# Kernel optimization log

Measured on AMD Instinct MI355X. Metric: run time of the kernel, lower is better.

Reference implementation:

```python
import jax, jax.numpy as jnp
import numpy as np

B, NF, G, H, W = 4, 64, 8, 96, 96
K, KK = 3, 9
CG = NF // G  # channels per deformable group


def _conv3(x, w, b):
    # 3x3 conv, stride 1, pad 1, NCHW/OIHW
    y = jax.lax.conv_general_dilated(x, w, (1, 1), ((1, 1), (1, 1)),
                                     dimension_numbers=('NCHW', 'OIHW', 'NCHW'))
    return y + b[None, :, None, None]


def _lrelu(x):
    return jnp.where(x >= 0, x, 0.1 * x)


def _up2(x):
    # bilinear x2 upsample, align_corners=False (PyTorch semantics: src clamped at 0, indices clamped at n-1)
    def up_axis(x, axis):
        n = x.shape[axis]
        src = jnp.maximum((jnp.arange(2 * n, dtype=jnp.float32) + 0.5) / 2.0 - 0.5, 0.0)
        i0 = jnp.floor(src).astype(jnp.int32)
        i1 = jnp.minimum(i0 + 1, n - 1)
        t = (src - i0.astype(jnp.float32))
        x0 = jnp.take(x, i0, axis=axis)
        x1 = jnp.take(x, i1, axis=axis)
        shp = [1] * x.ndim
        shp[axis] = 2 * n
        t = t.reshape(shp)
        return x0 * (1.0 - t) + x1 * t
    return up_axis(up_axis(x, 2), 3)


def _dcn(x, off_feat, w_om, b_om, w_d, b_d):
    # Modulated deformable conv (DCNv2, separate offset input), 3x3, stride 1, pad 1, dil 1,
    # conv groups = 1, deformable groups = G.
    b, c, h, w = x.shape
    om = _conv3(off_feat, w_om, b_om)                     # [B, 3*G*KK, H, W]
    o_y, o_x, m = jnp.split(om, 3, axis=1)                # each [B, G*KK, H, W]
    off_y = o_y.reshape(b, G, KK, h, w)
    off_x = o_x.reshape(b, G, KK, h, w)
    mask = jax.nn.sigmoid(m).reshape(b, G, KK, h, w)

    dy = (jnp.arange(KK, dtype=jnp.float32) // K - 1.0)   # [-1,-1,-1,0,0,0,1,1,1]
    dx = (jnp.arange(KK, dtype=jnp.float32) % K - 1.0)
    ys = jnp.arange(h, dtype=jnp.float32)
    xs = jnp.arange(w, dtype=jnp.float32)
    # sampling positions: [B, G, KK, H, W]
    py = off_y + ys[None, None, None, :, None] + dy[None, None, :, None, None]
    px = off_x + xs[None, None, None, None, :] + dx[None, None, :, None, None]

    y0f = jnp.floor(py); x0f = jnp.floor(px)
    ty = py - y0f; tx = px - x0f
    y0 = y0f.astype(jnp.int32); x0 = x0f.astype(jnp.int32)
    y1 = y0 + 1; x1 = x0 + 1

    xg = x.reshape(b, G, CG, h * w)  # per-deformable-group channels

    def samp(iy, ix):
        valid = ((iy >= 0) & (iy < h) & (ix >= 0) & (ix < w)).astype(x.dtype)  # [B,G,KK,H,W]
        idx = jnp.clip(iy, 0, h - 1) * w + jnp.clip(ix, 0, w - 1)
        idxf = idx.reshape(b, G, 1, KK * h * w)
        v = jnp.take_along_axis(xg, jnp.broadcast_to(idxf, (b, G, CG, KK * h * w)), axis=3)
        return v.reshape(b, G, CG, KK, h, w) * valid[:, :, None]

    w00 = ((1 - ty) * (1 - tx))[:, :, None]
    w01 = ((1 - ty) * tx)[:, :, None]
    w10 = (ty * (1 - tx))[:, :, None]
    w11 = (ty * tx)[:, :, None]
    cols = (samp(y0, x0) * w00 + samp(y0, x1) * w01 +
            samp(y1, x0) * w10 + samp(y1, x1) * w11)
    cols = cols * mask[:, :, None]                        # modulation
    cols = cols.reshape(b, c, KK, h, w)
    out = jnp.einsum('bckhw,ock->bohw', cols, w_d.reshape(c, c, KK))
    return out + b_d[None, :, None, None]


def setup_inputs() -> dict:
    key = jax.random.key(0)
    ks = jax.random.split(key, 20)
    s = 0.05
    inp = {
        'src0': jax.random.normal(ks[0], (B, NF, H, W), jnp.float32),
        'src1': jax.random.normal(ks[1], (B, NF, H, W), jnp.float32),
        'last_offset': jax.random.normal(ks[2], (B, NF, H // 2, W // 2), jnp.float32),
        'last_feature': jax.random.normal(ks[3], (B, NF, H // 2, W // 2), jnp.float32),
        'w_off1': jax.random.normal(ks[4], (NF, 2 * NF, 3, 3), jnp.float32) * s,
        'b_off1': jax.random.normal(ks[5], (NF,), jnp.float32) * s,
        'w_off2': jax.random.normal(ks[6], (NF, 2 * NF, 3, 3), jnp.float32) * s,
        'b_off2': jax.random.normal(ks[7], (NF,), jnp.float32) * s,
        'w_off3': jax.random.normal(ks[8], (NF, NF, 3, 3), jnp.float32) * s,
        'b_off3': jax.random.normal(ks[9], (NF,), jnp.float32) * s,
        'w_om': jax.random.normal(ks[10], (3 * G * KK, NF, 3, 3), jnp.float32) * s,
        'b_om': jax.random.normal(ks[11], (3 * G * KK,), jnp.float32) * s,
        'w_dcn': jax.random.normal(ks[12], (NF, NF, 3, 3), jnp.float32) * s,
        'b_dcn': jax.random.normal(ks[13], (NF,), jnp.float32) * s,
        'w_fea': jax.random.normal(ks[14], (NF, 2 * NF, 3, 3), jnp.float32) * s,
        'b_fea': jax.random.normal(ks[15], (NF,), jnp.float32) * s,
    }
    return inp


def reference(src0, src1, last_offset, last_feature,
              w_off1, b_off1, w_off2, b_off2, w_off3, b_off3,
              w_om, b_om, w_dcn, b_dcn, w_fea, b_fea):
    offset = _lrelu(_conv3(jnp.concatenate([src0, src1], axis=1), w_off1, b_off1))
    lo = _up2(last_offset)
    offset = _lrelu(_conv3(jnp.concatenate([offset, lo * 2.0], axis=1), w_off2, b_off2))
    offset = _lrelu(_conv3(offset, w_off3, b_off3))
    feature = _dcn(src0, offset, w_om, b_om, w_dcn, b_dcn)
    lf = _up2(last_feature)
    feature = _conv3(jnp.concatenate([feature, lf], axis=1), w_fea, b_fea)
    feature = _lrelu(feature)
    return (offset, feature)
```

## Files before the change

### kernel.cpp

```cpp
#include <hip/hip_runtime.h>
#include <hip/hip_fp16.h>
#include <math.h>

typedef __attribute__((ext_vector_type(8))) short bf16x8;
typedef __attribute__((ext_vector_type(8))) _Float16 half8;
typedef __attribute__((ext_vector_type(4))) float f32x4;
typedef __attribute__((ext_vector_type(4))) int int4v;

#define GL_LDS16(g, l) __builtin_amdgcn_global_load_lds( \
    (const __attribute__((address_space(1))) void*)(g), \
    (__attribute__((address_space(3))) void*)(l), 16, 0, 0)

__device__ __forceinline__ ushort f2bf(float f) {
    union { float f; unsigned u; } v; v.f = f;
    unsigned r = (v.u + 0x7fffu + ((v.u >> 16) & 1u)) >> 16;
    return (ushort)r;
}
__device__ __forceinline__ float bf2f(ushort h) {
    union { unsigned u; float f; } v; v.u = ((unsigned)h) << 16;
    return v.f;
}

__device__ __forceinline__ void prep_one(const float* __restrict__ w,
        ushort* __restrict__ wp, int u, int Cin, int CoutR, int CoutP) {
    int oc = u % CoutP; int t = u / CoutP;
    int kg = t & 3; t >>= 2;
    int kk = t % 9; int cc = t / 9;
    alignas(16) ushort tmp[8];
    for (int j = 0; j < 8; ++j) {
        int c = cc * 32 + kg * 8 + j;
        float v = (oc < CoutR) ? w[((size_t)oc * Cin + c) * 9 + kk] : 0.f;
        tmp[j] = f2bf(v);
    }
    *(int4v*)(wp + (size_t)u * 8) = *(int4v*)tmp;
}

__global__ __launch_bounds__(256) void pack_combo_k(
        const float* __restrict__ s0, const float* __restrict__ s1,
        const float* __restrict__ lo, const float* __restrict__ lf,
        const float* __restrict__ w1, const float* __restrict__ w2,
        const float* __restrict__ w3, const float* __restrict__ wom,
        const float* __restrict__ wd, const float* __restrict__ wf,
        const float* __restrict__ bom,
        ushort* __restrict__ xin1, ushort* __restrict__ xin2,
        ushort* __restrict__ xin4, ushort* __restrict__ xg1,
        ushort* __restrict__ w1p, ushort* __restrict__ w2p,
        ushort* __restrict__ w3p, ushort* __restrict__ womp,
        ushort* __restrict__ wdp, ushort* __restrict__ wfp,
        float* __restrict__ bpp, float* __restrict__ zg) {
    int b = blockIdx.y;
    int z = blockIdx.z;
    int px = blockIdx.x * 64 + (threadIdx.x & 63);
    int u = threadIdx.x >> 6;
    if (z == 0) {
        for (int half = 0; half < 2; ++half) {
            int cg = u + half * 4;
            float vals[16];
            alignas(16) ushort tmp[16];
            for (int i = 0; i < 16; ++i) {
                int c = cg * 16 + i;
                float v = (c < 64) ? s0[((size_t)(b * 64 + c)) * 9216 + px]
                                   : s1[((size_t)(b * 64 + c - 64)) * 9216 + px];
                vals[i] = v;
                tmp[i] = f2bf(v);
            }
            ushort* dst = xin1 + ((size_t)(b * 9216) + px) * 128 + cg * 16;
            *(int4v*)dst = *(int4v*)&tmp[0];
            *(int4v*)(dst + 8) = *(int4v*)&tmp[8];
            if (half == 0) {
                alignas(16) __half th[16];
                for (int i = 0; i < 16; ++i) th[i] = __float2half(vals[i]);
                ushort* gdst = xg1 + (((size_t)(b * 8 + cg * 2) * 9216) + px) * 8;
                *(int4v*)gdst = *(int4v*)&th[0];
                *(int4v*)(gdst + 9216 * 8) = *(int4v*)&th[8];
            }
        }
    } else if (z < 3) {
        const float* in = (z == 1) ? lo : lf;
        float scale = (z == 1) ? 2.0f : 1.0f;
        ushort* xo = (z == 1) ? xin2 : xin4;
        int y = px / 96, x = px % 96;
        float sy = fmaxf(y * 0.5f - 0.25f, 0.f);
        float sx = fmaxf(x * 0.5f - 0.25f, 0.f);
        int y0 = (int)sy, x0 = (int)sx;
        float ty = sy - (float)y0, tx = sx - (float)x0;
        int y1 = min(y0 + 1, 47), x1 = min(x0 + 1, 47);
        alignas(16) ushort tmp[16];
        for (int i = 0; i < 16; ++i) {
            int c = u * 16 + i;
            const float* p = in + ((size_t)(b * 64 + c)) * 2304;
            float v00 = p[y0 * 48 + x0], v01 = p[y0 * 48 + x1];
            float v10 = p[y1 * 48 + x0], v11 = p[y1 * 48 + x1];
            float v = (v00 * (1.f - tx) + v01 * tx) * (1.f - ty)
                    + (v10 * (1.f - tx) + v11 * tx) * ty;
            tmp[i] = f2bf(v * scale);
        }
        ushort* dst = xo + ((size_t)(b * 9216) + px) * 128 + 64 + u * 16;
        *(int4v*)dst = *(int4v*)&tmp[0];
        *(int4v*)(dst + 8) = *(int4v*)&tmp[8];
    } else {
        int uu = (blockIdx.x + 144 * blockIdx.y) * 256 + threadIdx.x;
        if (uu < 9216) prep_one(w1, w1p, uu, 128, 64, 64);
        else if (uu < 18432) prep_one(w2, w2p, uu - 9216, 128, 64, 64);
        else if (uu < 23040) prep_one(w3, w3p, uu - 18432, 64, 64, 64);
        else if (uu < 43776) {
            int v = uu - 23040;
            int ocp = v % 288; int t = v / 288;
            int kg = t & 3; t >>= 2;
            int kk = t % 9; int cc = t / 9;
            int t3 = ocp & 3, gkkp = ocp >> 2;
            alignas(16) ushort tmp[8];
            for (int j = 0; j < 8; ++j) {
                int c = cc * 32 + kg * 8 + j;
                float vv = (t3 < 3)
                    ? wom[((size_t)(t3 * 72 + gkkp) * 64 + c) * 9 + kk] : 0.f;
                tmp[j] = f2bf(vv);
            }
            *(int4v*)(womp + (size_t)v * 8) = *(int4v*)tmp;
        } else if (uu < 48384) {
            int v = uu - 43776;
            int oc = v & 63; int gkk = v >> 6;
            int g = gkk / 9, kk = gkk % 9;
            alignas(16) __half tmp[8];
            for (int j = 0; j < 8; ++j)
                tmp[j] = __float2half(wd[((size_t)oc * 64 + g * 8 + j) * 9 + kk]);
            *(int4v*)(wdp + (size_t)v * 8) = *(int4v*)tmp;
        } else if (uu < 57600) prep_one(wf, wfp, uu - 48384, 128, 64, 64);
        else if (uu < 57888) {
            int ocp = uu - 57600; int t3 = ocp & 3, gkkp = ocp >> 2;
            bpp[ocp] = (t3 < 3) ? bom[t3 * 72 + gkkp] : 0.f;
        } else if (uu < 57904) zg[uu - 57888] = 0.f;
    }
}

template<int CIN, int MT, int NZ, bool LRELU, bool ST_F32, bool ST_CHL>
__global__ __launch_bounds__(256, 4) void conv_mfma_k(
        const ushort* __restrict__ xin,
        const ushort* __restrict__ wp,
        const float* __restrict__ bias,
        float* __restrict__ outf,
        ushort* __restrict__ chl,
        const ushort* __restrict__ zg,
        int CoutR, int CoutP, int ochs, int ocoff) {
    constexpr int SL = CIN / 64;
    constexpr int OCN = MT * 16;
    __shared__ ushort s_act[SL][7200];

    int tid = threadIdx.x;
    int wv = tid >> 6, ln = tid & 63;
    int l15 = ln & 15, l4 = ln >> 4;

    constexpr int TOTAL = 144 * 4 * NZ;
    constexpr int CHUNK = TOTAL / 8;
    int bid = blockIdx.x;
    int nid = (bid & 7) * CHUNK + (bid >> 3);
    int zc = nid % NZ; int r1 = nid / NZ;
    int tile = r1 % 144; int b = r1 / 144;
    int bx = (tile % 12) * 8, by = (tile / 12) * 8;
    int oc0 = zc * OCN;

    int px_l = wv * 16 + l15;
    int py = px_l >> 3, pxx = px_l & 7;
    int b_base = (py * 10 + pxx) * 72 + l4 * 8;

    const ushort* wlane = wp + ((size_t)l4 * CoutP + oc0 + l15) * 8;

    f32x4 acc[MT];
#pragma unroll
    for (int mt = 0; mt < MT; ++mt) acc[mt] = (f32x4){0.f, 0.f, 0.f, 0.f};

    auto STAGE = [&](int sl, int buf) {
        for (int i = tid; i < 900; i += 256) {
            int p = i / 9, q = i - p * 9;
            int gy = by + (p / 10) - 1, gx = bx + (p % 10) - 1;
            const ushort* src = zg;
            if (q < 8 && (unsigned)gy < 96u && (unsigned)gx < 96u)
                src = xin + ((size_t)(b * 9216 + gy * 96 + gx) * CIN
                             + sl * 64 + q * 8);
            GL_LDS16(src, s_act[buf] + (size_t)i * 8);
        }
    };

    STAGE(0, 0);
    __syncthreads();
#pragma unroll
    for (int sl = 0; sl < SL; ++sl) {
        if (sl + 1 < SL) STAGE(sl + 1, (sl + 1) & 1);
#pragma unroll
        for (int cc2 = 0; cc2 < 2; ++cc2) {
#pragma unroll
            for (int kk = 0; kk < 9; ++kk) {
                bf16x8 bfrag = *(const bf16x8*)(s_act[sl & (SL - 1)] + b_base +
                                   ((kk / 3) * 10 + (kk % 3)) * 72 + cc2 * 32);
#pragma unroll
                for (int mt = 0; mt < MT; ++mt) {
                    bf16x8 af = *(const bf16x8*)(wlane +
                        ((size_t)((sl * 2 + cc2) * 36 + kk * 4) * CoutP + mt * 16) * 8);
                    acc[mt] = __builtin_amdgcn_mfma_f32_16x16x32_bf16(
                        af, bfrag, acc[mt], 0, 0, 0);
                }
            }
        }
        if (sl + 1 < SL) __syncthreads();
    }

    int gy = by + py, gx = bx + pxx;
    size_t pxg = (size_t)b * 9216 + gy * 96 + gx;
#pragma unroll
    for (int mt = 0; mt < MT; ++mt) {
        int ocb = oc0 + mt * 16 + l4 * 4;
        ushort hb[4];
#pragma unroll
        for (int r = 0; r < 4; ++r) {
            int oc = ocb + r;
            float v = acc[mt][r] + ((oc < CoutR) ? bias[oc] : 0.f);
            if (LRELU) v = (v >= 0.f) ? v : 0.1f * v;
            hb[r] = f2bf(v);
            if (ST_F32 && oc < CoutR)
                outf[((size_t)b * CoutR + oc) * 9216 + gy * 96 + gx] = v;
        }
        if (ST_CHL && ocb < CoutR) {
            uint2 pk;
            pk.x = (uint)hb[0] | ((uint)hb[1] << 16);
            pk.y = (uint)hb[2] | ((uint)hb[3] << 16);
            *(uint2*)(chl + pxg * ochs + ocoff + ocb) = pk;
        }
    }
}

__global__ __launch_bounds__(128, 4) void dcn_fused_k(
        const ushort* __restrict__ xg1,
        const ushort* __restrict__ om,
        const ushort* __restrict__ wdp,
        const float* __restrict__ bd, ushort* __restrict__ chl) {
    __shared__ float s_red[64][17];
    int tid = threadIdx.x;
    int kq = tid >> 6, ln = tid & 63;
    int l15 = ln & 15, l4 = ln >> 4;
    int bid = blockIdx.x;
    int nid = (bid & 7) * 288 + (bid >> 3);
    int pxb = nid % 576; int b = nid / 576;
    int px = pxb * 16 + l15;
    int y = px / 96, xx = px % 96;

    f32x4 acc[4];
#pragma unroll
    for (int mt = 0; mt < 4; ++mt) acc[mt] = (f32x4){0.f, 0.f, 0.f, 0.f};
    const ushort* omp_ = om + ((size_t)b * 9216 + px) * 288 + kq * 144;

    uint2 ovv[9];
#pragma unroll
    for (int s = 0; s < 9; ++s)
        ovv[s] = *(const uint2*)(omp_ + s * 16 + l4 * 4);

    int4v Abuf[2][4];
    float cwbuf[2][4];

    auto PREP = [&](int s, int4v* A, float* cw) {
        int gkk = kq * 36 + s * 4 + l4;
        int g = gkk / 9, kk = gkk - g * 9;
        union { uint2 u; ushort us[4]; } ov; ov.u = ovv[s];
        float oy = bf2f(ov.us[0]), ox = bf2f(ov.us[1]);
        float mm = 1.f / (1.f + __expf(-bf2f(ov.us[2])));
        float py = oy + (float)(y + kk / 3 - 1);
        float pxf = ox + (float)(xx + kk % 3 - 1);
        float yf = floorf(py), xf = floorf(pxf);
        float fy = py - yf, fx = pxf - xf;
        int iy0 = (int)yf, ix0 = (int)xf;
        int iy1 = iy0 + 1, ix1 = ix0 + 1;
        float vy0 = ((unsigned)iy0 < 96u) ? 1.f : 0.f;
        float vy1 = ((unsigned)iy1 < 96u) ? 1.f : 0.f;
        float vx0 = ((unsigned)ix0 < 96u) ? 1.f : 0.f;
        float vx1 = ((unsigned)ix1 < 96u) ? 1.f : 0.f;
        int r0 = min(max(iy0, 0), 95), r1 = min(max(iy1, 0), 95);
        int lb = min(max(ix0, 0), 94);
        float h0 = (float)min(max(ix0 - lb, 0), 1);
        float h1 = (float)min(max(ix1 - lb, 0), 1);
        float wx0 = (1.f - fx) * vx0, wx1 = fx * vx1;
        float xw0 = wx0 * (1.f - h0) + wx1 * (1.f - h1);
        float xw1 = wx0 * h0 + wx1 * h1;
        float rw0 = (1.f - fy) * vy0 * mm, rw1 = fy * vy1 * mm;
        cw[0] = rw0 * xw0; cw[1] = rw0 * xw1;
        cw[2] = rw1 * xw0; cw[3] = rw1 * xw1;
        const ushort* gp = xg1 + ((size_t)(b * 8 + g) * 9216) * 8;
        const ushort* p0 = gp + ((size_t)(r0 * 96 + lb)) * 8;
        const ushort* p1 = gp + ((size_t)(r1 * 96 + lb)) * 8;
        A[0] = *(const int4v*)p0;
        A[1] = *(const int4v*)(p0 + 8);
        A[2] = *(const int4v*)p1;
        A[3] = *(const int4v*)(p1 + 8);
    };

    PREP(0, Abuf[0], cwbuf[0]);
#pragma unroll
    for (int s = 0; s < 9; ++s) {
        if (s + 1 < 9) PREP(s + 1, Abuf[(s + 1) & 1], cwbuf[(s + 1) & 1]);
        const int4v* A = Abuf[s & 1];
        const float* cw = cwbuf[s & 1];
        union { int4v v; __half2 h2[4]; } a0, a1, b0, b1;
        a0.v = A[0]; a1.v = A[1]; b0.v = A[2]; b1.v = A[3];
        __half2 w0 = __float2half2_rn(cw[0]);
        __half2 w1 = __float2half2_rn(cw[1]);
        __half2 w2 = __float2half2_rn(cw[2]);
        __half2 w3 = __float2half2_rn(cw[3]);
        union { __half2 h2[4]; half8 v; } bu;
#pragma unroll
        for (int j = 0; j < 4; ++j) {
            __half2 t = __hmul2(a0.h2[j], w0);
            t = __hfma2(a1.h2[j], w1, t);
            t = __hfma2(b0.h2[j], w2, t);
            t = __hfma2(b1.h2[j], w3, t);
            bu.h2[j] = t;
        }
        int gkk = kq * 36 + s * 4 + l4;
#pragma unroll
        for (int mt = 0; mt < 4; ++mt) {
            half8 af = *(const half8*)(wdp +
                ((size_t)gkk * 64 + mt * 16 + l15) * 8);
            acc[mt] = __builtin_amdgcn_mfma_f32_16x16x32_f16(
                af, bu.v, acc[mt], 0, 0, 0);
        }
    }

    if (kq) {
#pragma unroll
        for (int mt = 0; mt < 4; ++mt)
#pragma unroll
            for (int r = 0; r < 4; ++r)
                s_red[ln][mt * 4 + r] = acc[mt][r];
    }
    __syncthreads();
    if (!kq) {
        size_t pb = (size_t)b * 9216 + px;
#pragma unroll
        for (int mt = 0; mt < 4; ++mt) {
            ushort hb[4];
#pragma unroll
            for (int r = 0; r < 4; ++r) {
                int oc = mt * 16 + l4 * 4 + r;
                float v = acc[mt][r] + s_red[ln][mt * 4 + r] + bd[oc];
                hb[r] = f2bf(v);
            }
            uint2 pk;
            pk.x = (uint)hb[0] | ((uint)hb[1] << 16);
            pk.y = (uint)hb[2] | ((uint)hb[3] << 16);
            *(uint2*)(chl + pb * 128 + mt * 16 + l4 * 4) = pk;
        }
    }
}

extern "C" void kernel_launch(void* const* d_in, const int* in_sizes, int n_in,
                              void* d_out, int out_size, void* d_ws, size_t ws_size,
                              hipStream_t stream) {
    const float* src0  = (const float*)d_in[0];
    const float* src1  = (const float*)d_in[1];
    const float* l_off = (const float*)d_in[2];
    const float* l_fea = (const float*)d_in[3];
    const float* w1 = (const float*)d_in[4];   const float* b1 = (const float*)d_in[5];
    const float* w2 = (const float*)d_in[6];   const float* b2 = (const float*)d_in[7];
    const float* w3 = (const float*)d_in[8];   const float* b3 = (const float*)d_in[9];
    const float* wom = (const float*)d_in[10]; const float* bom = (const float*)d_in[11];
    const float* wd = (const float*)d_in[12];  const float* bd = (const float*)d_in[13];
    const float* wf = (const float*)d_in[14];  const float* bf = (const float*)d_in[15];

    char* W = (char*)d_ws;
    ushort* xin1 = (ushort*)(W + 0);
    ushort* xin2 = (ushort*)(W + 9437184);
    ushort* xoff = (ushort*)(W + 9437184);
    ushort* xin3 = (ushort*)(W + 18874368);
    ushort* omb  = (ushort*)(W + 23592960);
    ushort* xin4 = (ushort*)(W + 44826624);
    ushort* xg1  = (ushort*)(W + 54263808);
    ushort* w1p  = (ushort*)(W + 58982400);
    ushort* w2p  = (ushort*)(W + 59129856);
    ushort* w3p  = (ushort*)(W + 59277312);
    ushort* womp = (ushort*)(W + 59351040);
    ushort* wdp  = (ushort*)(W + 59682816);
    ushort* wfp  = (ushort*)(W + 59756544);
    float*  bpp  = (float*)(W + 59904000);
    float*  zgrd = (float*)(W + 59905152);

    float* out_off = (float*)d_out;
    float* out_fea = out_off + (size_t)4 * 64 * 9216;

    pack_combo_k<<<dim3(144, 4, 4), 256, 0, stream>>>(
        src0, src1, l_off, l_fea, w1, w2, w3, wom, wd, wf, bom,
        xin1, xin2, xin4, xg1, w1p, w2p, w3p, womp, wdp, wfp, bpp, zgrd);

    const ushort* zg = (const ushort*)zgrd;
    conv_mfma_k<128, 2, 2, true, false, true><<<1152, 256, 0, stream>>>(
        xin1, w1p, b1, nullptr, xin2, zg, 64, 64, 128, 0);
    conv_mfma_k<128, 2, 2, true, false, true><<<1152, 256, 0, stream>>>(
        xin2, w2p, b2, nullptr, xin3, zg, 64, 64, 64, 0);
    conv_mfma_k<64, 2, 2, true, true, true><<<1152, 256, 0, stream>>>(
        xin3, w3p, b3, out_off, xoff, zg, 64, 64, 64, 0);
    conv_mfma_k<64, 6, 3, false, false, true><<<1728, 256, 0, stream>>>(
        xoff, womp, bpp, nullptr, omb, zg, 288, 288, 288, 0);
    dcn_fused_k<<<2304, 128, 0, stream>>>(xg1, omb, wdp, bd, xin4);
    conv_mfma_k<128, 2, 2, true, true, false><<<1152, 256, 0, stream>>>(
        xin4, wfp, bf, out_fea, nullptr, zg, 64, 64, 0, 0);
}
```

Measured before the change: 145.1 us.

## Fuse offset/mask conv into deformable conv kernel, drop om intermediate

Removes the separate conv that produced the 288-channel offset/mask tensor. Each DCN block now stages its 3x18 halo of the offset features into LDS and computes the offsets and masks with MFMA before sampling. This saves one kernel launch plus the write and re-read of the large om buffer. In exchange, weights are read from global memory per block with no reuse across blocks, register pressure rises (launch bounds cut to 3 blocks), and the per-block compute grows.

New measurement: 131.8 us. 9.2% less time.

```diff
diff --git a/kernel.cpp b/kernel.cpp
--- a/kernel.cpp
+++ b/kernel.cpp
@@ -228,11 +228,15 @@
     }
 }
 
-__global__ __launch_bounds__(128, 4) void dcn_fused_k(
+__global__ __launch_bounds__(128, 3) void dcn_fused_k(
+        const ushort* __restrict__ xoff,
         const ushort* __restrict__ xg1,
-        const ushort* __restrict__ om,
+        const ushort* __restrict__ womp,
+        const float* __restrict__ bpp,
         const ushort* __restrict__ wdp,
-        const float* __restrict__ bd, ushort* __restrict__ chl) {
+        const float* __restrict__ bd, ushort* __restrict__ chl,
+        const ushort* __restrict__ zg) {
+    __shared__ ushort s_x[3456];
     __shared__ float s_red[64][17];
     int tid = threadIdx.x;
     int kq = tid >> 6, ln = tid & 63;
@@ -240,18 +244,48 @@
     int bid = blockIdx.x;
     int nid = (bid & 7) * 288 + (bid >> 3);
     int pxb = nid % 576; int b = nid / 576;
-    int px = pxb * 16 + l15;
-    int y = px / 96, xx = px % 96;
+    int px0 = pxb * 16;
+    int px = px0 + l15;
+    int y = px0 / 96, x0 = px0 % 96;
+    int xx = x0 + l15;
+
+    for (int i = tid; i < 432; i += 128) {
+        int P = i >> 3, s8 = i & 7;
+        int q = s8 ^ (P & 7);
+        int ry = y - 1 + P / 18, rx = x0 - 1 + P % 18;
+        const ushort* src = zg;
+        if ((unsigned)ry < 96u && (unsigned)rx < 96u)
+            src = xoff + (((size_t)b * 9216 + ry * 96 + rx) * 64 + q * 8);
+        GL_LDS16(src, s_x + (size_t)i * 8);
+    }
+    __syncthreads();
+
+    f32x4 aom[9];
+#pragma unroll
+    for (int s = 0; s < 9; ++s) aom[s] = (f32x4){0.f, 0.f, 0.f, 0.f};
+#pragma unroll
+    for (int kk = 0; kk < 9; ++kk) {
+        int ky = kk / 3, kx = kk % 3;
+#pragma unroll
+        for (int cc = 0; cc < 2; ++cc) {
+            int P = ky * 18 + l15 + kx;
+            int c8 = cc * 4 + l4;
+            bf16x8 bfrag = *(const bf16x8*)(s_x +
+                ((size_t)(P * 8 + (c8 ^ (P & 7)))) * 8);
+#pragma unroll
+            for (int s = 0; s < 9; ++s) {
+                bf16x8 af = *(const bf16x8*)(womp +
+                    ((size_t)(((cc * 9 + kk) * 4 + l4) * 288)
+                     + kq * 144 + s * 16 + l15) * 8);
+                aom[s] = __builtin_amdgcn_mfma_f32_16x16x32_bf16(
+                    af, bfrag, aom[s], 0, 0, 0);
+            }
+        }
+    }
 
     f32x4 acc[4];
 #pragma unroll
     for (int mt = 0; mt < 4; ++mt) acc[mt] = (f32x4){0.f, 0.f, 0.f, 0.f};
-    const ushort* omp_ = om + ((size_t)b * 9216 + px) * 288 + kq * 144;
-
-    uint2 ovv[9];
-#pragma unroll
-    for (int s = 0; s < 9; ++s)
-        ovv[s] = *(const uint2*)(omp_ + s * 16 + l4 * 4);
 
     int4v Abuf[2][4];
     float cwbuf[2][4];
@@ -259,9 +293,10 @@
     auto PREP = [&](int s, int4v* A, float* cw) {
         int gkk = kq * 36 + s * 4 + l4;
         int g = gkk / 9, kk = gkk - g * 9;
-        union { uint2 u; ushort us[4]; } ov; ov.u = ovv[s];
-        float oy = bf2f(ov.us[0]), ox = bf2f(ov.us[1]);
-        float mm = 1.f / (1.f + __expf(-bf2f(ov.us[2])));
+        int bofs = kq * 144 + s * 16 + l4 * 4;
+        float oy = aom[s][0] + bpp[bofs];
+        float ox = aom[s][1] + bpp[bofs + 1];
+        float mm = 1.f / (1.f + __expf(-(aom[s][2] + bpp[bofs + 2])));
         float py = oy + (float)(y + kk / 3 - 1);
         float pxf = ox + (float)(xx + kk % 3 - 1);
         float yf = floorf(py), xf = floorf(pxf);
@@ -368,7 +403,6 @@
     ushort* xin2 = (ushort*)(W + 9437184);
     ushort* xoff = (ushort*)(W + 9437184);
     ushort* xin3 = (ushort*)(W + 18874368);
-    ushort* omb  = (ushort*)(W + 23592960);
     ushort* xin4 = (ushort*)(W + 44826624);
     ushort* xg1  = (ushort*)(W + 54263808);
     ushort* w1p  = (ushort*)(W + 58982400);
@@ -394,9 +428,8 @@
         xin2, w2p, b2, nullptr, xin3, zg, 64, 64, 64, 0);
     conv_mfma_k<64, 2, 2, true, true, true><<<1152, 256, 0, stream>>>(
         xin3, w3p, b3, out_off, xoff, zg, 64, 64, 64, 0);
-    conv_mfma_k<64, 6, 3, false, false, true><<<1728, 256, 0, stream>>>(
-        xoff, womp, bpp, nullptr, omb, zg, 288, 288, 288, 0);
-    dcn_fused_k<<<2304, 128, 0, stream>>>(xg1, omb, wdp, bd, xin4);
+    dcn_fused_k<<<2304, 128, 0, stream>>>(xoff, xg1, womp, bpp, wdp, bd,
+                                          xin4, zg);
     conv_mfma_k<128, 2, 2, true, true, false><<<1152, 256, 0, stream>>>(
         xin4, wfp, bf, out_fea, nullptr, zg, 64, 64, 0, 0);
 }
```
